# Performance work log

Hardware: AMD Instinct MI355X
Metric: run time of the kernel (lower is better)

Reference implementation:

```python
import jax, jax.numpy as jnp
import numpy as np


def setup_inputs() -> dict:
    key = jax.random.key(0)
    ks = jax.random.split(key, 6)
    B, S, H, HD = 2, 2048, 2048, 128
    scale = 0.02
    return {
        "hidden_state": jax.random.normal(ks[0], (B, S, H), jnp.float32),
        "attention_mask": jnp.ones((B, 1, 1, S), jnp.int32),
        "Wq": jax.random.normal(ks[1], (H, H), jnp.float32) * scale,
        "bq": jnp.zeros((H,), jnp.float32),
        "Wk": jax.random.normal(ks[2], (HD, H), jnp.float32) * scale,
        "bk": jnp.zeros((HD,), jnp.float32),
        "Wv": jax.random.normal(ks[3], (HD, H), jnp.float32) * scale,
        "bv": jnp.zeros((HD,), jnp.float32),
        "Wo": jax.random.normal(ks[4], (H, H), jnp.float32) * scale,
        "bo": jnp.zeros((H,), jnp.float32),
    }


def reference(hidden_state, attention_mask, Wq, bq, Wk, bk, Wv, bv, Wo, bo):
    B, S, H = hidden_state.shape
    hd = Wk.shape[0]          # head_dim (single shared KV head)
    nh = H // hd              # num query heads
    # projections (torch Linear: x @ W.T + b)
    q = (hidden_state @ Wq.T + bq).reshape(B, S, nh, hd).transpose(0, 2, 1, 3)  # (B,nh,S,hd)
    k = hidden_state @ Wk.T + bk   # (B,S,hd) shared head
    v = hidden_state @ Wv.T + bv   # (B,S,hd)
    scores = jnp.einsum('bhqd,bkd->bhqk', q, k) / jnp.sqrt(jnp.float32(hd))
    scores = jnp.where(attention_mask == 0, -jnp.inf, scores)
    probs = jax.nn.softmax(scores, axis=-1)
    # dropout p=0.0 -> identity (inference)
    out = jnp.einsum('bhqk,bkd->bhqd', probs, v)           # (B,nh,S,hd)
    out = out.transpose(0, 2, 1, 3).reshape(B, S, H)
    return out @ Wo.T + bo
```

## Files before the change

### kernel.cpp

```cpp
#include <hip/hip_runtime.h>

typedef unsigned short u16;
typedef unsigned int u32;
typedef __attribute__((ext_vector_type(8))) short bf16x8;
typedef __attribute__((ext_vector_type(4))) float f32x4;
typedef __attribute__((ext_vector_type(16))) float f32x16;

#define QSC 0.12751798f

__device__ __forceinline__ u16 f2bf(float f) {
  union { float f; unsigned u; } a; a.f = f;
  unsigned r = a.u + 0x7fffu + ((a.u >> 16) & 1u);
  return (u16)(r >> 16);
}

__device__ __forceinline__ void gload16(const void* g, void* l) {
  __builtin_amdgcn_global_load_lds(
      (const __attribute__((address_space(1))) unsigned int*)g,
      (__attribute__((address_space(3))) unsigned int*)l, 16, 0, 0);
}

__global__ __launch_bounds__(256) void cvt_k(const float* __restrict__ src,
                                             u16* __restrict__ dst, int n4) {
  int i = blockIdx.x * 256 + threadIdx.x;
  if (i >= n4) return;
  float4 v = ((const float4*)src)[i];
  ushort4 o;
  o.x = f2bf(v.x); o.y = f2bf(v.y); o.z = f2bf(v.z); o.w = f2bf(v.w);
  ((ushort4*)dst)[i] = o;
}

template <int MODE>
__global__ __launch_bounds__(256) void gemm_bt_k(
    const u16* __restrict__ A, const u16* __restrict__ Bm,
    const float* __restrict__ bias0, const float* __restrict__ bias1,
    const float* __restrict__ bias2,
    float* __restrict__ outF, u16* __restrict__ outQ,
    u16* __restrict__ outK, u16* __restrict__ outVt,
    int M, int N, int K) {
  __shared__ u16 As[128 * 32];
  __shared__ u16 Bs[128 * 32];
  const int t = threadIdx.x;
  const int lane = t & 63, wid = t >> 6;
  const int m0 = blockIdx.y * 128, n0 = blockIdx.x * 128;
  const int wr = (wid >> 1) * 64, wc = (wid & 1) * 64;
  const int col = lane & 15, grp = lane >> 4;

  const int srow = t >> 2;
  const int sp = t & 3;
  const int sslot = (sp ^ ((srow >> 1) & 3)) * 8;
  const u16* aS0 = A + (size_t)(m0 + srow) * K + sslot;
  const u16* aS1 = A + (size_t)(m0 + srow + 64) * K + sslot;
  const u16* bS0 = Bm + (size_t)(n0 + srow) * K + sslot;
  const u16* bS1 = Bm + (size_t)(n0 + srow + 64) * K + sslot;
  u16* aD0 = As + t * 8; u16* aD1 = As + (256 + t) * 8;
  u16* bD0 = Bs + t * 8; u16* bD1 = Bs + (256 + t) * 8;

  f32x4 acc[4][4] = {};
  const int nk = K >> 5;
  for (int kt = 0; kt < nk; ++kt) {
    __syncthreads();
    const int ko = kt * 32;
    gload16(aS0 + ko, aD0);
    gload16(aS1 + ko, aD1);
    gload16(bS0 + ko, bD0);
    gload16(bS1 + ko, bD1);
    __syncthreads();
    bf16x8 af[4], bfr[4];
#pragma unroll
    for (int f = 0; f < 4; ++f) {
      int ra = wr + f * 16 + col;
      af[f] = *(const bf16x8*)(const void*)((const char*)As + ra * 64 +
                                            ((grp ^ ((ra >> 1) & 3)) << 4));
      int rb = wc + f * 16 + col;
      bfr[f] = *(const bf16x8*)(const void*)((const char*)Bs + rb * 64 +
                                             ((grp ^ ((rb >> 1) & 3)) << 4));
    }
    __builtin_amdgcn_s_setprio(1);
#pragma unroll
    for (int i = 0; i < 4; ++i)
#pragma unroll
      for (int j = 0; j < 4; ++j)
        acc[i][j] = __builtin_amdgcn_mfma_f32_16x16x32_bf16(af[i], bfr[j],
                                                            acc[i][j], 0, 0, 0);
    __builtin_amdgcn_s_setprio(0);
  }

#pragma unroll
  for (int i = 0; i < 4; ++i) {
    const int gmb = m0 + wr + i * 16 + grp * 4;
#pragma unroll
    for (int j = 0; j < 4; ++j) {
      const int gn = n0 + wc + j * 16 + col;
      float bv;
      if (MODE == 1) bv = bias0[gn];
      else bv = (gn < 2048) ? bias0[gn]
                            : (gn < 2176 ? bias1[gn - 2048] : bias2[gn - 2176]);
#pragma unroll
      for (int r = 0; r < 4; ++r) {
        const int gm = gmb + r;
        float val = acc[i][j][r] + bv;
        if (MODE == 1) {
          outF[(size_t)gm * N + gn] = val;
        } else {
          if (gn < 2048) {
            outQ[(size_t)gm * 2048 + gn] = f2bf(val * QSC);
          } else if (gn < 2176) {
            outK[(size_t)gm * 128 + (gn - 2048)] = f2bf(val);
          } else {
            const int b = gm >> 11, s = gm & 2047, d = gn - 2176;
            outVt[((size_t)(b * 128 + d) << 11) + s] = f2bf(val);
          }
        }
      }
    }
  }
}

__global__ __launch_bounds__(256, 2) void attn_k(const u16* __restrict__ Q,
                                                 const u16* __restrict__ Kb,
                                                 const u16* __restrict__ Vt,
                                                 u16* __restrict__ O) {
  __shared__ u16 Ks[2][64 * 128];
  __shared__ u16 Vs[2][128 * 64];
  const int t = threadIdx.x, lane = t & 63, w = t >> 6;
  const int qt = blockIdx.x & 15;
  const int h = (blockIdx.x >> 4) & 15;
  const int b = blockIdx.x >> 8;
  const int l31 = lane & 31, hi = lane >> 5;
  const int swl = l31 & 7;
  const int q0w = qt * 128 + w * 32;

  bf16x8 qf[8];
  {
    const u16* qp = Q + (size_t)(b * 2048 + q0w + l31) * 2048 + h * 128 + hi * 8;
#pragma unroll
    for (int kc = 0; kc < 8; ++kc) qf[kc] = *(const bf16x8*)(qp + kc * 16);
  }

  f32x16 of[4] = {};
  float mrun = -3e38f, lsum = 0.f;

  const int krow = t >> 4, kslot = t & 15;
  const int sig = (krow & 3) | ((krow & 4) << 1) | ((krow & 8) >> 1);
  const int vrow = t >> 3, vslot = t & 7;
  const u16* ksrc[4];
  const u16* vsrc[4];
#pragma unroll
  for (int i = 0; i < 4; ++i) {
    ksrc[i] = Kb + (size_t)(b * 2048 + i * 16 + sig) * 128 + ((kslot ^ (krow & 7)) * 8);
    vsrc[i] = Vt + (size_t)(b * 128 + i * 32 + vrow) * 2048 + ((vslot ^ (vrow & 7)) * 8);
  }
  const int ldst = t * 8;

  auto STAGE = [&](int ktn, int nb) {
#pragma unroll
    for (int i = 0; i < 4; ++i) {
      gload16(ksrc[i] + ktn * 8192, &Ks[nb][i * 2048 + ldst]);
      gload16(vsrc[i] + ktn * 64, &Vs[nb][i * 2048 + ldst]);
    }
  };

  STAGE(0, 0);
  __syncthreads();
  int bb = 0;
  for (int kt = 0; kt < 32; ++kt) {
    if (kt < 31) STAGE(kt + 1, bb ^ 1);
    const char* kbase = (const char*)Ks[bb];
    const char* vbase = (const char*)Vs[bb];

    f32x16 st0 = {}, st1 = {};
    __builtin_amdgcn_s_setprio(1);
#pragma unroll
    for (int kc = 0; kc < 8; ++kc) {
      const int sw = ((kc * 2 + hi) ^ swl) << 4;
      bf16x8 k0 = *(const bf16x8*)(const void*)(kbase + l31 * 256 + sw);
      bf16x8 k1 = *(const bf16x8*)(const void*)(kbase + (32 + l31) * 256 + sw);
      st0 = __builtin_amdgcn_mfma_f32_32x32x16_bf16(k0, qf[kc], st0, 0, 0, 0);
      st1 = __builtin_amdgcn_mfma_f32_32x32x16_bf16(k1, qf[kc], st1, 0, 0, 0);
    }
    __builtin_amdgcn_s_setprio(0);

    float mx = fmaxf(st0[0], st1[0]);
#pragma unroll
    for (int i = 1; i < 16; ++i) mx = fmaxf(mx, fmaxf(st0[i], st1[i]));
    mx = fmaxf(mx, __shfl_xor(mx, 32));

    if (__any(mx > mrun + 8.f)) {
      float mnew = fmaxf(mrun, mx);
      float al = __builtin_amdgcn_exp2f(mrun - mnew);
      mrun = mnew;
      lsum *= al;
#pragma unroll
      for (int rr = 0; rr < 16; ++rr) {
        const int rho = (rr & 3) + 8 * (rr >> 2) + 4 * hi;
        float av = __shfl(al, (lane & 32) | rho);
#pragma unroll
        for (int dt = 0; dt < 4; ++dt) of[dt][rr] *= av;
      }
    }

    u32 pk0[8], pk1[8];
    float ps = 0.f;
#pragma unroll
    for (int a = 0; a < 8; ++a) {
      float e0 = __builtin_amdgcn_exp2f(st0[2 * a] - mrun);
      float e1 = __builtin_amdgcn_exp2f(st0[2 * a + 1] - mrun);
      float e2 = __builtin_amdgcn_exp2f(st1[2 * a] - mrun);
      float e3 = __builtin_amdgcn_exp2f(st1[2 * a + 1] - mrun);
      ps += (e0 + e1) + (e2 + e3);
      asm("v_cvt_pk_bf16_f32 %0, %1, %2" : "=v"(pk0[a]) : "v"(e0), "v"(e1));
      asm("v_cvt_pk_bf16_f32 %0, %1, %2" : "=v"(pk1[a]) : "v"(e2), "v"(e3));
    }
    lsum += ps;

    __builtin_amdgcn_s_setprio(1);
#pragma unroll
    for (int kvc = 0; kvc < 4; ++kvc) {
      union { u32 u[4]; bf16x8 v; } pu;
#pragma unroll
      for (int ww = 0; ww < 4; ++ww)
        pu.u[ww] = (kvc >= 2) ? pk1[(kvc & 1) * 4 + ww] : pk0[(kvc & 1) * 4 + ww];
      const int swv = ((kvc * 2 + hi) ^ swl) << 4;
#pragma unroll
      for (int dt = 0; dt < 4; ++dt) {
        bf16x8 vb = *(const bf16x8*)(const void*)(vbase + (dt * 32 + l31) * 128 + swv);
        of[dt] = __builtin_amdgcn_mfma_f32_32x32x16_bf16(pu.v, vb, of[dt], 0, 0, 0);
      }
    }
    __builtin_amdgcn_s_setprio(0);

    __syncthreads();
    bb ^= 1;
  }

  float lt = lsum + __shfl_xor(lsum, 32);
  float inv = 1.0f / lt;
#pragma unroll
  for (int rr = 0; rr < 16; ++rr) {
    const int rho = (rr & 3) + 8 * (rr >> 2) + 4 * hi;
    float iv = __shfl(inv, (lane & 32) | rho);
    u16* orow = O + (size_t)(b * 2048 + q0w + rho) * 2048 + h * 128 + l31;
#pragma unroll
    for (int dt = 0; dt < 4; ++dt) orow[dt * 32] = f2bf(of[dt][rr] * iv);
  }
}

extern "C" void kernel_launch(void* const* d_in, const int* in_sizes, int n_in,
                              void* d_out, int out_size, void* d_ws,
                              size_t ws_size, hipStream_t stream) {
  const float* hidden = (const float*)d_in[0];
  const float* Wq = (const float*)d_in[2];
  const float* bq = (const float*)d_in[3];
  const float* Wk = (const float*)d_in[4];
  const float* bk = (const float*)d_in[5];
  const float* Wv = (const float*)d_in[6];
  const float* bv = (const float*)d_in[7];
  const float* Wo = (const float*)d_in[8];
  const float* bo = (const float*)d_in[9];
  float* out = (float*)d_out;

  char* ws = (char*)d_ws;
  u16* hid  = (u16*)(ws);
  u16* wqkv = (u16*)(ws + 16777216);
  u16* wo   = (u16*)(ws + 26214400);
  u16* q    = (u16*)(ws + 34603008);
  u16* kb   = (u16*)(ws + 51380224);
  u16* vt   = (u16*)(ws + 52428800);
  u16* attn = (u16*)(ws + 53477376);

  cvt_k<<<8192, 256, 0, stream>>>(hidden, hid, 2097152);
  cvt_k<<<4096, 256, 0, stream>>>(Wq, wqkv, 1048576);
  cvt_k<<<256, 256, 0, stream>>>(Wk, wqkv + 2048 * 2048, 65536);
  cvt_k<<<256, 256, 0, stream>>>(Wv, wqkv + 2176 * 2048, 65536);
  cvt_k<<<4096, 256, 0, stream>>>(Wo, wo, 1048576);

  gemm_bt_k<0><<<dim3(18, 32), 256, 0, stream>>>(
      hid, wqkv, bq, bk, bv, nullptr, q, kb, vt, 4096, 2304, 2048);

  attn_k<<<512, 256, 0, stream>>>(q, kb, vt, attn);

  gemm_bt_k<1><<<dim3(16, 32), 256, 0, stream>>>(
      attn, wo, bo, nullptr, nullptr, out, nullptr, nullptr, nullptr,
      4096, 2048, 2048);
}
```

Baseline: 216.5 us.

## Software-pipeline QK^T of next tile with PV of current tile; merge conversion kernels

The attention loop is restructured so the QK^T MFMAs for tile t+1 are issued alongside the PV MFMAs for tile t, while the softmax exp work for tile t runs between them. K and V loads are now staged separately, each on its own schedule, with a peeled prologue and epilogue. This is meant to hide softmax latency and the LDS load waits behind matrix work. Separately, five fp32-to-bf16 conversion launches are merged into one kernel to cut launch overhead. The cost is more live registers (two score accumulators plus packed probabilities), which may lower occupancy.

```diff
diff --git a/kernel.cpp b/kernel.cpp
--- a/kernel.cpp
+++ b/kernel.cpp
@@ -20,14 +20,32 @@
       (__attribute__((address_space(3))) unsigned int*)l, 16, 0, 0);
 }
 
-__global__ __launch_bounds__(256) void cvt_k(const float* __restrict__ src,
-                                             u16* __restrict__ dst, int n4) {
+__global__ __launch_bounds__(256) void cvt_all_k(
+    const float* __restrict__ h, const float* __restrict__ wq,
+    const float* __restrict__ wk, const float* __restrict__ wv,
+    const float* __restrict__ wo, u16* __restrict__ hid,
+    u16* __restrict__ wqkv, u16* __restrict__ wob) {
   int i = blockIdx.x * 256 + threadIdx.x;
-  if (i >= n4) return;
-  float4 v = ((const float4*)src)[i];
+  if (i >= 4325376) return;
+  const float4* s;
+  ushort4* d;
+  if (i < 2097152) {
+    s = (const float4*)h + i;              d = (ushort4*)hid + i;
+  } else if (i < 3145728) {
+    s = (const float4*)wq + (i - 2097152); d = (ushort4*)wqkv + (i - 2097152);
+  } else if (i < 3211264) {
+    s = (const float4*)wk + (i - 3145728);
+    d = (ushort4*)(wqkv + 4194304) + (i - 3145728);
+  } else if (i < 3276800) {
+    s = (const float4*)wv + (i - 3211264);
+    d = (ushort4*)(wqkv + 4456448) + (i - 3211264);
+  } else {
+    s = (const float4*)wo + (i - 3276800); d = (ushort4*)wob + (i - 3276800);
+  }
+  float4 v = *s;
   ushort4 o;
   o.x = f2bf(v.x); o.y = f2bf(v.y); o.z = f2bf(v.z); o.w = f2bf(v.w);
-  ((ushort4*)dst)[i] = o;
+  *d = o;
 }
 
 template <int MODE>
@@ -138,54 +156,54 @@
     for (int kc = 0; kc < 8; ++kc) qf[kc] = *(const bf16x8*)(qp + kc * 16);
   }
 
-  f32x16 of[4] = {};
-  float mrun = -3e38f, lsum = 0.f;
-
   const int krow = t >> 4, kslot = t & 15;
   const int sig = (krow & 3) | ((krow & 4) << 1) | ((krow & 8) >> 1);
   const int vrow = t >> 3, vslot = t & 7;
-  const u16* ksrc[4];
-  const u16* vsrc[4];
-#pragma unroll
-  for (int i = 0; i < 4; ++i) {
-    ksrc[i] = Kb + (size_t)(b * 2048 + i * 16 + sig) * 128 + ((kslot ^ (krow & 7)) * 8);
-    vsrc[i] = Vt + (size_t)(b * 128 + i * 32 + vrow) * 2048 + ((vslot ^ (vrow & 7)) * 8);
-  }
+  const u16* ksrc0 =
+      Kb + (size_t)(b * 2048 + sig) * 128 + ((kslot ^ (krow & 7)) * 8);
+  const u16* vsrc0 =
+      Vt + (size_t)(b * 128 + vrow) * 2048 + ((vslot ^ (vrow & 7)) * 8);
   const int ldst = t * 8;
 
-  auto STAGE = [&](int ktn, int nb) {
-#pragma unroll
-    for (int i = 0; i < 4; ++i) {
-      gload16(ksrc[i] + ktn * 8192, &Ks[nb][i * 2048 + ldst]);
-      gload16(vsrc[i] + ktn * 64, &Vs[nb][i * 2048 + ldst]);
-    }
+  auto STAGE_K = [&](int ktn, int nb) {
+#pragma unroll
+    for (int i = 0; i < 4; ++i)
+      gload16(ksrc0 + i * 2048 + ktn * 8192, &Ks[nb][i * 2048 + ldst]);
   };
-
-  STAGE(0, 0);
+  auto STAGE_V = [&](int ktn, int nb) {
+#pragma unroll
+    for (int i = 0; i < 4; ++i)
+      gload16(vsrc0 + (size_t)i * 65536 + ktn * 64, &Vs[nb][i * 2048 + ldst]);
+  };
+
+  STAGE_K(0, 0);
+  STAGE_V(0, 0);
+  STAGE_K(1, 1);
   __syncthreads();
-  int bb = 0;
-  for (int kt = 0; kt < 32; ++kt) {
-    if (kt < 31) STAGE(kt + 1, bb ^ 1);
-    const char* kbase = (const char*)Ks[bb];
-    const char* vbase = (const char*)Vs[bb];
-
-    f32x16 st0 = {}, st1 = {};
-    __builtin_amdgcn_s_setprio(1);
-#pragma unroll
-    for (int kc = 0; kc < 8; ++kc) {
-      const int sw = ((kc * 2 + hi) ^ swl) << 4;
-      bf16x8 k0 = *(const bf16x8*)(const void*)(kbase + l31 * 256 + sw);
-      bf16x8 k1 = *(const bf16x8*)(const void*)(kbase + (32 + l31) * 256 + sw);
-      st0 = __builtin_amdgcn_mfma_f32_32x32x16_bf16(k0, qf[kc], st0, 0, 0, 0);
-      st1 = __builtin_amdgcn_mfma_f32_32x32x16_bf16(k1, qf[kc], st1, 0, 0, 0);
-    }
-    __builtin_amdgcn_s_setprio(0);
+
+  f32x16 st0 = {}, st1 = {};
+#pragma unroll
+  for (int kc = 0; kc < 8; ++kc) {
+    const int sw = ((kc * 2 + hi) ^ swl) << 4;
+    bf16x8 k0 = *(const bf16x8*)(const void*)((const char*)Ks[0] + l31 * 256 + sw);
+    bf16x8 k1 = *(const bf16x8*)(const void*)((const char*)Ks[0] + (32 + l31) * 256 + sw);
+    st0 = __builtin_amdgcn_mfma_f32_32x32x16_bf16(k0, qf[kc], st0, 0, 0, 0);
+    st1 = __builtin_amdgcn_mfma_f32_32x32x16_bf16(k1, qf[kc], st1, 0, 0, 0);
+  }
+  STAGE_V(1, 1);
+  __syncthreads();
+
+  f32x16 of[4] = {};
+  float mrun = -3e38f, lsum = 0.f;
+  u32 pk[4][4];
+
+  for (int tt = 0; tt < 31; ++tt) {
+    if (tt < 30) STAGE_K(tt + 2, tt & 1);
 
     float mx = fmaxf(st0[0], st1[0]);
 #pragma unroll
     for (int i = 1; i < 16; ++i) mx = fmaxf(mx, fmaxf(st0[i], st1[i]));
     mx = fmaxf(mx, __shfl_xor(mx, 32));
-
     if (__any(mx > mrun + 8.f)) {
       float mnew = fmaxf(mrun, mx);
       float al = __builtin_amdgcn_exp2f(mrun - mnew);
@@ -199,8 +217,71 @@
         for (int dt = 0; dt < 4; ++dt) of[dt][rr] *= av;
       }
     }
-
-    u32 pk0[8], pk1[8];
+    {
+      float ps = 0.f;
+#pragma unroll
+      for (int a = 0; a < 8; ++a) {
+        float e0 = __builtin_amdgcn_exp2f(st0[2 * a] - mrun);
+        float e1 = __builtin_amdgcn_exp2f(st0[2 * a + 1] - mrun);
+        float e2 = __builtin_amdgcn_exp2f(st1[2 * a] - mrun);
+        float e3 = __builtin_amdgcn_exp2f(st1[2 * a + 1] - mrun);
+        ps += (e0 + e1) + (e2 + e3);
+        asm("v_cvt_pk_bf16_f32 %0, %1, %2" : "=v"(pk[a >> 2][a & 3]) : "v"(e0), "v"(e1));
+        asm("v_cvt_pk_bf16_f32 %0, %1, %2" : "=v"(pk[2 + (a >> 2)][a & 3]) : "v"(e2), "v"(e3));
+      }
+      lsum += ps;
+    }
+
+    const char* kbase = (const char*)Ks[(tt + 1) & 1];
+    const char* vbase = (const char*)Vs[tt & 1];
+    f32x16 n0 = {}, n1 = {};
+    __builtin_amdgcn_s_setprio(1);
+#pragma unroll
+    for (int kc = 0; kc < 8; ++kc) {
+      const int sw = ((kc * 2 + hi) ^ swl) << 4;
+      bf16x8 k0 = *(const bf16x8*)(const void*)(kbase + l31 * 256 + sw);
+      bf16x8 k1 = *(const bf16x8*)(const void*)(kbase + (32 + l31) * 256 + sw);
+      n0 = __builtin_amdgcn_mfma_f32_32x32x16_bf16(k0, qf[kc], n0, 0, 0, 0);
+      n1 = __builtin_amdgcn_mfma_f32_32x32x16_bf16(k1, qf[kc], n1, 0, 0, 0);
+    }
+#pragma unroll
+    for (int kvc = 0; kvc < 4; ++kvc) {
+      union { u32 u[4]; bf16x8 v; } pu;
+#pragma unroll
+      for (int ww = 0; ww < 4; ++ww) pu.u[ww] = pk[kvc][ww];
+      const int swv = ((kvc * 2 + hi) ^ swl) << 4;
+#pragma unroll
+      for (int dt = 0; dt < 4; ++dt) {
+        bf16x8 vb = *(const bf16x8*)(const void*)(vbase + (dt * 32 + l31) * 128 + swv);
+        of[dt] = __builtin_amdgcn_mfma_f32_32x32x16_bf16(pu.v, vb, of[dt], 0, 0, 0);
+      }
+    }
+    __builtin_amdgcn_s_setprio(0);
+
+    __syncthreads();
+    if (tt < 30) STAGE_V(tt + 2, tt & 1);
+    st0 = n0;
+    st1 = n1;
+  }
+
+  {
+    float mx = fmaxf(st0[0], st1[0]);
+#pragma unroll
+    for (int i = 1; i < 16; ++i) mx = fmaxf(mx, fmaxf(st0[i], st1[i]));
+    mx = fmaxf(mx, __shfl_xor(mx, 32));
+    if (__any(mx > mrun + 8.f)) {
+      float mnew = fmaxf(mrun, mx);
+      float al = __builtin_amdgcn_exp2f(mrun - mnew);
+      mrun = mnew;
+      lsum *= al;
+#pragma unroll
+      for (int rr = 0; rr < 16; ++rr) {
+        const int rho = (rr & 3) + 8 * (rr >> 2) + 4 * hi;
+        float av = __shfl(al, (lane & 32) | rho);
+#pragma unroll
+        for (int dt = 0; dt < 4; ++dt) of[dt][rr] *= av;
+      }
+    }
     float ps = 0.f;
 #pragma unroll
     for (int a = 0; a < 8; ++a) {
@@ -209,18 +290,17 @@
       float e2 = __builtin_amdgcn_exp2f(st1[2 * a] - mrun);
       float e3 = __builtin_amdgcn_exp2f(st1[2 * a + 1] - mrun);
       ps += (e0 + e1) + (e2 + e3);
-      asm("v_cvt_pk_bf16_f32 %0, %1, %2" : "=v"(pk0[a]) : "v"(e0), "v"(e1));
-      asm("v_cvt_pk_bf16_f32 %0, %1, %2" : "=v"(pk1[a]) : "v"(e2), "v"(e3));
+      asm("v_cvt_pk_bf16_f32 %0, %1, %2" : "=v"(pk[a >> 2][a & 3]) : "v"(e0), "v"(e1));
+      asm("v_cvt_pk_bf16_f32 %0, %1, %2" : "=v"(pk[2 + (a >> 2)][a & 3]) : "v"(e2), "v"(e3));
     }
     lsum += ps;
-
+    const char* vbase = (const char*)Vs[1];
     __builtin_amdgcn_s_setprio(1);
 #pragma unroll
     for (int kvc = 0; kvc < 4; ++kvc) {
       union { u32 u[4]; bf16x8 v; } pu;
 #pragma unroll
-      for (int ww = 0; ww < 4; ++ww)
-        pu.u[ww] = (kvc >= 2) ? pk1[(kvc & 1) * 4 + ww] : pk0[(kvc & 1) * 4 + ww];
+      for (int ww = 0; ww < 4; ++ww) pu.u[ww] = pk[kvc][ww];
       const int swv = ((kvc * 2 + hi) ^ swl) << 4;
 #pragma unroll
       for (int dt = 0; dt < 4; ++dt) {
@@ -229,9 +309,6 @@
       }
     }
     __builtin_amdgcn_s_setprio(0);
-
-    __syncthreads();
-    bb ^= 1;
   }
 
   float lt = lsum + __shfl_xor(lsum, 32);
@@ -269,11 +346,7 @@
   u16* vt   = (u16*)(ws + 52428800);
   u16* attn = (u16*)(ws + 53477376);
 
-  cvt_k<<<8192, 256, 0, stream>>>(hidden, hid, 2097152);
-  cvt_k<<<4096, 256, 0, stream>>>(Wq, wqkv, 1048576);
-  cvt_k<<<256, 256, 0, stream>>>(Wk, wqkv + 2048 * 2048, 65536);
-  cvt_k<<<256, 256, 0, stream>>>(Wv, wqkv + 2176 * 2048, 65536);
-  cvt_k<<<4096, 256, 0, stream>>>(Wo, wo, 1048576);
+  cvt_all_k<<<16896, 256, 0, stream>>>(hidden, Wq, Wk, Wv, Wo, hid, wqkv, wo);
 
   gemm_bt_k<0><<<dim3(18, 32), 256, 0, stream>>>(
       hid, wqkv, bq, bk, bv, nullptr, q, kb, vt, 4096, 2304, 2048);
```

Result: faster. 212.0 us (-2.1%).
